# Kernel optimization log

Hardware: AMD Instinct MI355X
Metric: run time of the kernel (lower is better)

## Reference

```python
import jax, jax.numpy as jnp
import numpy as np

D_HID = 512          # RAECell output dim (nn.Linear(1024, 512))
DEPTH = 16           # internal levels -> 2**16 leaves, 131071 nodes


def _levels(left, right, leaf, root):
    """Group internal nodes by depth via host-side BFS (tree topology is static)."""
    levels = []
    frontier = [int(root)]
    while frontier:
        internal = [n for n in frontier if not leaf[n]]
        if internal:
            levels.append(np.asarray(internal, dtype=np.int32))
        frontier = [c for n in internal for c in (int(left[n]), int(right[n]))]
    return levels


def setup_inputs() -> dict:
    key = jax.random.key(0)
    n_leaves = 2 ** DEPTH
    n_nodes = 2 * n_leaves - 1
    first_leaf = n_leaves - 1
    idx = np.arange(n_nodes)
    # complete binary tree in heap layout
    left = np.where(idx < first_leaf, 2 * idx + 1, 0).astype(np.int64)
    right = np.where(idx < first_leaf, 2 * idx + 2, 0).astype(np.int64)
    is_leaf = (idx >= first_leaf).astype(np.int64)
    k1, k2, k3 = jax.random.split(key, 3)
    inp = jax.random.normal(k1, (n_nodes, D_HID), jnp.float32)
    W = jax.random.normal(k2, (D_HID, 2 * D_HID), jnp.float32) * (1.0 / np.sqrt(2 * D_HID))
    b = jax.random.normal(k3, (D_HID,), jnp.float32) * 0.01
    return {
        "left": jnp.asarray(left),
        "right": jnp.asarray(right),
        "is_leaf": jnp.asarray(is_leaf),
        "inp": inp,
        "root": 0,
        "W": W,
        "b": b,
    }


def reference(left, right, is_leaf, inp, root, W, b):
    # Tree indices are static -> pull to host once and batch the recursion
    # level-by-level (replaces the Python recursion + per-node tiny kernels
    # of the original with log2(N) batched concat+GEMM+tanh steps).
    l = np.asarray(left)
    r = np.asarray(right)
    leaf = np.asarray(is_leaf).astype(bool)
    levels = _levels(l, r, leaf, root)
    H = inp  # [n_nodes, 512]; leaf rows are the inputs, internal rows get overwritten bottom-up
    for lvl in reversed(levels):
        a = H[l[lvl]]              # [m, 512] left children
        c = H[r[lvl]]              # [m, 512] right children
        x = jnp.concatenate([a, c], axis=1)          # [m, 1024] == torch.cat((a, b))
        H = H.at[jnp.asarray(lvl)].set(jnp.tanh(x @ W.T + b))
    return H[int(root)]
```

## Files before the change

kernel.cpp:

```cpp
#include <hip/hip_runtime.h>
#include <hip/hip_fp16.h>

typedef _Float16 half8 __attribute__((ext_vector_type(8)));
typedef float f32x4 __attribute__((ext_vector_type(4)));

#define KDIM 1024
#define NDIM 512

#define GLOAD_LDS16(g, l) __builtin_amdgcn_global_load_lds(                 \
    (const __attribute__((address_space(1))) void*)(g),                     \
    (__attribute__((address_space(3))) void*)(l), 16, 0, 0)

__global__ __launch_bounds__(256, 2)
void rae_level_gemm_h(const _Float16* __restrict__ X, const _Float16* __restrict__ Wh,
                      const float* __restrict__ bias, _Float16* __restrict__ Yh)
{
    __shared__ _Float16 Xs[128 * 64];
    __shared__ _Float16 Ws[128 * 64];

    const int tid  = threadIdx.x;
    const int lane = tid & 63;
    const int wave = tid >> 6;
    const int wm = wave >> 1;
    const int wn = wave & 1;
    const int lrow = lane & 15;
    const int lq   = lane >> 4;

    const int brow = blockIdx.x * 128;
    const int bcol = blockIdx.y * 128;

    const int sr = tid >> 3;
    const int su = (((tid & 7) ^ (sr & 7)) << 3);

    const _Float16* xbase = X  + (size_t)(brow + sr) * KDIM + su;
    const _Float16* wbase = Wh + (size_t)(bcol + sr) * KDIM + su;

    f32x4 acc[4][4] = {};

    for (int k0 = 0; k0 < KDIM; k0 += 64) {
        __syncthreads();
        GLOAD_LDS16(xbase + k0,             Xs + tid * 8);
        GLOAD_LDS16(xbase + k0 + 32 * KDIM, Xs + tid * 8 + 2048);
        GLOAD_LDS16(xbase + k0 + 64 * KDIM, Xs + tid * 8 + 4096);
        GLOAD_LDS16(xbase + k0 + 96 * KDIM, Xs + tid * 8 + 6144);
        GLOAD_LDS16(wbase + k0,             Ws + tid * 8);
        GLOAD_LDS16(wbase + k0 + 32 * KDIM, Ws + tid * 8 + 2048);
        GLOAD_LDS16(wbase + k0 + 64 * KDIM, Ws + tid * 8 + 4096);
        GLOAD_LDS16(wbase + k0 + 96 * KDIM, Ws + tid * 8 + 6144);
        __syncthreads();

        #pragma unroll
        for (int ks = 0; ks < 2; ++ks) {
            half8 af[4], bf[4];
            #pragma unroll
            for (int i = 0; i < 4; ++i) {
                const int R = wm * 64 + i * 16 + lrow;
                const int phys = (ks * 4 + lq) ^ (R & 7);
                af[i] = *(const half8*)&Xs[R * 64 + phys * 8];
            }
            #pragma unroll
            for (int j = 0; j < 4; ++j) {
                const int R = wn * 64 + j * 16 + lrow;
                const int phys = (ks * 4 + lq) ^ (R & 7);
                bf[j] = *(const half8*)&Ws[R * 64 + phys * 8];
            }
            #pragma unroll
            for (int i = 0; i < 4; ++i)
                #pragma unroll
                for (int j = 0; j < 4; ++j)
                    acc[i][j] = __builtin_amdgcn_mfma_f32_16x16x32_f16(af[i], bf[j], acc[i][j], 0, 0, 0);
        }
    }

    #pragma unroll
    for (int j = 0; j < 4; ++j) {
        const int col = bcol + wn * 64 + j * 16 + lrow;
        const float bv = bias[col];
        #pragma unroll
        for (int i = 0; i < 4; ++i) {
            const int rbase = brow + wm * 64 + i * 16 + lq * 4;
            #pragma unroll
            for (int r = 0; r < 4; ++r)
                Yh[(size_t)(rbase + r) * NDIM + col] = (_Float16)tanhf(acc[i][j][r] + bv);
        }
    }
}

__device__ __forceinline__ void grid_barrier(unsigned* bar, unsigned nb)
{
    __syncthreads();
    if (threadIdx.x == 0) {
        __threadfence();
        unsigned* cnt = bar;
        unsigned* gen = bar + 32;
        unsigned g = __hip_atomic_load(gen, __ATOMIC_RELAXED, __HIP_MEMORY_SCOPE_AGENT);
        if (__hip_atomic_fetch_add(cnt, 1u, __ATOMIC_ACQ_REL, __HIP_MEMORY_SCOPE_AGENT) == nb - 1u) {
            __hip_atomic_store(cnt, 0u, __ATOMIC_RELAXED, __HIP_MEMORY_SCOPE_AGENT);
            __hip_atomic_store(gen, g + 1u, __ATOMIC_RELEASE, __HIP_MEMORY_SCOPE_AGENT);
        } else {
            while (__hip_atomic_load(gen, __ATOMIC_RELAXED, __HIP_MEMORY_SCOPE_AGENT) == g) {}
        }
        __threadfence();
    }
    __syncthreads();
}

#define TAIL_BK 256
#define TLD 264

__global__ __launch_bounds__(256, 1)
void rae_tail(const _Float16* __restrict__ Wh, const float* __restrict__ bias,
              _Float16* __restrict__ Hh, float* __restrict__ out,
              unsigned* __restrict__ bar)
{
    __shared__ _Float16 Xs[128 * TLD];
    __shared__ _Float16 Ws[64 * TLD];

    const int tid  = threadIdx.x;
    const int lane = tid & 63;
    const int wave = tid >> 6;
    const int lrow = lane & 15;
    const int lq   = lane >> 4;
    const int col0 = blockIdx.x * 64;

    const _Float16* wbase = Wh + (size_t)(col0 + (tid >> 2)) * KDIM + (size_t)((tid & 3) * 64);
    _Float16* wlds = Ws + (tid >> 2) * TLD + (tid & 3) * 64;

    const int xrow = tid >> 1;
    const int xseg = (tid & 1) * 128;

    for (int d = 7; d >= 0; --d) {
        const int m = 1 << d;
        const _Float16* X = Hh + (size_t)((2 << d) - 1) * NDIM;
        _Float16* Y = Hh + (size_t)((1 << d) - 1) * NDIM;

        f32x4 acc[2][4] = {};

        for (int k0 = 0; k0 < KDIM; k0 += TAIL_BK) {
            __syncthreads();
            {
                const _Float16* g = wbase + k0;
                #pragma unroll
                for (int j = 0; j < 8; ++j)
                    *(half8*)(wlds + j * 8) = *(const half8*)(g + j * 8);
            }
            if (xrow < m) {
                const _Float16* g = X + (size_t)xrow * KDIM + k0 + xseg;
                _Float16* l = Xs + xrow * TLD + xseg;
                #pragma unroll
                for (int j = 0; j < 16; ++j)
                    *(half8*)(l + j * 8) = *(const half8*)(g + j * 8);
            }
            __syncthreads();

            if (wave * 32 < m) {
                #pragma unroll
                for (int ks = 0; ks < TAIL_BK; ks += 32) {
                    half8 af[2], bf[4];
                    #pragma unroll
                    for (int i = 0; i < 2; ++i)
                        af[i] = *(const half8*)&Xs[(wave * 32 + i * 16 + lrow) * TLD + ks + lq * 8];
                    #pragma unroll
                    for (int j = 0; j < 4; ++j)
                        bf[j] = *(const half8*)&Ws[(j * 16 + lrow) * TLD + ks + lq * 8];
                    #pragma unroll
                    for (int i = 0; i < 2; ++i)
                        #pragma unroll
                        for (int j = 0; j < 4; ++j)
                            acc[i][j] = __builtin_amdgcn_mfma_f32_16x16x32_f16(af[i], bf[j], acc[i][j], 0, 0, 0);
                }
            }
        }

        if (wave * 32 < m) {
            #pragma unroll
            for (int j = 0; j < 4; ++j) {
                const int col = col0 + j * 16 + lrow;
                const float bv = bias[col];
                #pragma unroll
                for (int i = 0; i < 2; ++i) {
                    const int rbase = wave * 32 + i * 16 + lq * 4;
                    #pragma unroll
                    for (int r = 0; r < 4; ++r) {
                        const int row = rbase + r;
                        if (row < m) {
                            const float v = tanhf(acc[i][j][r] + bv);
                            if (d == 0) out[col] = v;
                            else Y[(size_t)row * NDIM + col] = (_Float16)v;
                        }
                    }
                }
            }
        }
        grid_barrier(bar, 8);
    }
}

__global__ void convert_w(const float* __restrict__ W, _Float16* __restrict__ Wh)
{
    const int i = blockIdx.x * 256 + threadIdx.x;
    const float4 v = ((const float4*)W)[i];
    _Float16 o[4] = {(_Float16)v.x, (_Float16)v.y, (_Float16)v.z, (_Float16)v.w};
    *(float2*)(Wh + (size_t)i * 4) = *(float2*)o;
}

__global__ void convert_leaves(const float* __restrict__ inp, _Float16* __restrict__ Hh)
{
    const size_t i = (size_t)blockIdx.x * 256 + threadIdx.x;
    const float4 v = ((const float4*)(inp + (size_t)65535 * NDIM))[i];
    _Float16 o[4] = {(_Float16)v.x, (_Float16)v.y, (_Float16)v.z, (_Float16)v.w};
    *(float2*)(Hh + (size_t)65535 * NDIM + i * 4) = *(float2*)o;
}

extern "C" void kernel_launch(void* const* d_in, const int* in_sizes, int n_in,
                              void* d_out, int out_size, void* d_ws, size_t ws_size,
                              hipStream_t stream)
{
    const float* inp  = (const float*)d_in[3];
    const float* W    = (const float*)d_in[5];
    const float* bias = (const float*)d_in[6];
    float* out = (float*)d_out;

    _Float16* Wh  = (_Float16*)d_ws;
    unsigned* bar = (unsigned*)((char*)d_ws + (1 << 20));
    _Float16* Hh  = (_Float16*)((char*)d_ws + (2 << 20));

    hipMemsetAsync(bar, 0, 256, stream);
    convert_w<<<512, 256, 0, stream>>>(W, Wh);
    convert_leaves<<<32768, 256, 0, stream>>>(inp, Hh);

    for (int d = 15; d >= 8; --d) {
        const int m = 1 << d;
        const _Float16* Xp = Hh + (size_t)((2 << d) - 1) * NDIM;
        _Float16* Yp = Hh + (size_t)((1 << d) - 1) * NDIM;
        rae_level_gemm_h<<<dim3(m / 128, 4), 256, 0, stream>>>(Xp, Wh, bias, Yp);
    }

    rae_tail<<<8, 256, 0, stream>>>(Wh, bias, Hh, out, bar);
}
```

Measured before the change: 675.1 us.

## Fuse leaf fp32 conversion into first level GEMM and widen persistent tail

Removes the separate leaf conversion kernel: the deepest level now reads fp32 leaves directly, converting them to fp16 on the way into LDS. This avoids writing and re-reading 64K fp16 rows. The persistent tail kernel now starts at depth 10 with 32 blocks instead of 8. It keeps a full 64-column strip of W resident in LDS and reads activations straight from global memory, which removes three GEMM launches. The costs are synchronous non-async X loads in the first level and more grid-barrier participants with little parallel work per level.

```diff
diff --git a/kernel.cpp b/kernel.cpp
--- a/kernel.cpp
+++ b/kernel.cpp
@@ -86,6 +86,89 @@
     }
 }
 
+__global__ __launch_bounds__(256, 2)
+void rae_level15_f32(const float* __restrict__ Xf, const _Float16* __restrict__ Wh,
+                     const float* __restrict__ bias, _Float16* __restrict__ Yh)
+{
+    __shared__ _Float16 Xs[128 * 64];
+    __shared__ _Float16 Ws[128 * 64];
+
+    const int tid  = threadIdx.x;
+    const int lane = tid & 63;
+    const int wave = tid >> 6;
+    const int wm = wave >> 1;
+    const int wn = wave & 1;
+    const int lrow = lane & 15;
+    const int lq   = lane >> 4;
+
+    const int brow = blockIdx.x * 128;
+    const int bcol = blockIdx.y * 128;
+
+    const int sr = tid >> 3;
+    const int su = (((tid & 7) ^ (sr & 7)) << 3);
+
+    const float*    xbase = Xf + (size_t)(brow + sr) * KDIM + su;
+    const _Float16* wbase = Wh + (size_t)(bcol + sr) * KDIM + su;
+
+    f32x4 acc[4][4] = {};
+
+    for (int k0 = 0; k0 < KDIM; k0 += 64) {
+        __syncthreads();
+        GLOAD_LDS16(wbase + k0,             Ws + tid * 8);
+        GLOAD_LDS16(wbase + k0 + 32 * KDIM, Ws + tid * 8 + 2048);
+        GLOAD_LDS16(wbase + k0 + 64 * KDIM, Ws + tid * 8 + 4096);
+        GLOAD_LDS16(wbase + k0 + 96 * KDIM, Ws + tid * 8 + 6144);
+        #pragma unroll
+        for (int c = 0; c < 4; ++c) {
+            const float4* g = (const float4*)(xbase + k0 + (size_t)c * 32 * KDIM);
+            const float4 aa = g[0];
+            const float4 bb = g[1];
+            half8 h;
+            h[0] = (_Float16)aa.x; h[1] = (_Float16)aa.y;
+            h[2] = (_Float16)aa.z; h[3] = (_Float16)aa.w;
+            h[4] = (_Float16)bb.x; h[5] = (_Float16)bb.y;
+            h[6] = (_Float16)bb.z; h[7] = (_Float16)bb.w;
+            *(half8*)(Xs + tid * 8 + c * 2048) = h;
+        }
+        __syncthreads();
+
+        #pragma unroll
+        for (int ks = 0; ks < 2; ++ks) {
+            half8 af[4], bf[4];
+            #pragma unroll
+            for (int i = 0; i < 4; ++i) {
+                const int R = wm * 64 + i * 16 + lrow;
+                const int phys = (ks * 4 + lq) ^ (R & 7);
+                af[i] = *(const half8*)&Xs[R * 64 + phys * 8];
+            }
+            #pragma unroll
+            for (int j = 0; j < 4; ++j) {
+                const int R = wn * 64 + j * 16 + lrow;
+                const int phys = (ks * 4 + lq) ^ (R & 7);
+                bf[j] = *(const half8*)&Ws[R * 64 + phys * 8];
+            }
+            #pragma unroll
+            for (int i = 0; i < 4; ++i)
+                #pragma unroll
+                for (int j = 0; j < 4; ++j)
+                    acc[i][j] = __builtin_amdgcn_mfma_f32_16x16x32_f16(af[i], bf[j], acc[i][j], 0, 0, 0);
+        }
+    }
+
+    #pragma unroll
+    for (int j = 0; j < 4; ++j) {
+        const int col = bcol + wn * 64 + j * 16 + lrow;
+        const float bv = bias[col];
+        #pragma unroll
+        for (int i = 0; i < 4; ++i) {
+            const int rbase = brow + wm * 64 + i * 16 + lq * 4;
+            #pragma unroll
+            for (int r = 0; r < 4; ++r)
+                Yh[(size_t)(rbase + r) * NDIM + col] = (_Float16)tanhf(acc[i][j][r] + bv);
+        }
+    }
+}
+
 __device__ __forceinline__ void grid_barrier(unsigned* bar, unsigned nb)
 {
     __syncthreads();
@@ -105,94 +188,91 @@
     __syncthreads();
 }
 
-#define TAIL_BK 256
-#define TLD 264
+#define TWLD 1032
+
+template<int NF>
+__device__ __forceinline__ void tail_level(
+    int d, const _Float16* __restrict__ Hh, float* __restrict__ out,
+    const float* __restrict__ bias, const _Float16* Ws,
+    int col0, int wstrip, int lrow, int lq, _Float16* __restrict__ Y)
+{
+    const int m = 1 << d;
+    const _Float16* X = Hh + ((size_t)(2 << d) - 1) * NDIM;
+    const int rbase0 = wstrip * (NF * 16);
+    if (NF == 1 && rbase0 >= m) return;
+
+    f32x4 acc[NF][4] = {};
+
+    #pragma unroll
+    for (int ks = 0; ks < 32; ++ks) {
+        half8 af[NF], bf[4];
+        #pragma unroll
+        for (int i = 0; i < NF; ++i)
+            af[i] = *(const half8*)(X + (size_t)(rbase0 + i * 16 + lrow) * KDIM + ks * 32 + lq * 8);
+        #pragma unroll
+        for (int j = 0; j < 4; ++j)
+            bf[j] = *(const half8*)(Ws + (j * 16 + lrow) * TWLD + ks * 32 + lq * 8);
+        #pragma unroll
+        for (int i = 0; i < NF; ++i)
+            #pragma unroll
+            for (int j = 0; j < 4; ++j)
+                acc[i][j] = __builtin_amdgcn_mfma_f32_16x16x32_f16(af[i], bf[j], acc[i][j], 0, 0, 0);
+    }
+
+    #pragma unroll
+    for (int j = 0; j < 4; ++j) {
+        const int col = col0 + j * 16 + lrow;
+        const float bv = bias[col];
+        #pragma unroll
+        for (int i = 0; i < NF; ++i) {
+            #pragma unroll
+            for (int r = 0; r < 4; ++r) {
+                const int row = rbase0 + i * 16 + lq * 4 + r;
+                if (row < m) {
+                    const float v = tanhf(acc[i][j][r] + bv);
+                    if (d == 0) out[col] = v;
+                    else Y[(size_t)row * NDIM + col] = (_Float16)v;
+                }
+            }
+        }
+    }
+}
 
 __global__ __launch_bounds__(256, 1)
 void rae_tail(const _Float16* __restrict__ Wh, const float* __restrict__ bias,
               _Float16* __restrict__ Hh, float* __restrict__ out,
               unsigned* __restrict__ bar)
 {
-    __shared__ _Float16 Xs[128 * TLD];
-    __shared__ _Float16 Ws[64 * TLD];
+    __shared__ _Float16 Ws[64 * TWLD];
 
     const int tid  = threadIdx.x;
     const int lane = tid & 63;
     const int wave = tid >> 6;
     const int lrow = lane & 15;
     const int lq   = lane >> 4;
-    const int col0 = blockIdx.x * 64;
-
-    const _Float16* wbase = Wh + (size_t)(col0 + (tid >> 2)) * KDIM + (size_t)((tid & 3) * 64);
-    _Float16* wlds = Ws + (tid >> 2) * TLD + (tid & 3) * 64;
-
-    const int xrow = tid >> 1;
-    const int xseg = (tid & 1) * 128;
-
-    for (int d = 7; d >= 0; --d) {
-        const int m = 1 << d;
-        const _Float16* X = Hh + (size_t)((2 << d) - 1) * NDIM;
-        _Float16* Y = Hh + (size_t)((1 << d) - 1) * NDIM;
-
-        f32x4 acc[2][4] = {};
-
-        for (int k0 = 0; k0 < KDIM; k0 += TAIL_BK) {
-            __syncthreads();
-            {
-                const _Float16* g = wbase + k0;
-                #pragma unroll
-                for (int j = 0; j < 8; ++j)
-                    *(half8*)(wlds + j * 8) = *(const half8*)(g + j * 8);
-            }
-            if (xrow < m) {
-                const _Float16* g = X + (size_t)xrow * KDIM + k0 + xseg;
-                _Float16* l = Xs + xrow * TLD + xseg;
-                #pragma unroll
-                for (int j = 0; j < 16; ++j)
-                    *(half8*)(l + j * 8) = *(const half8*)(g + j * 8);
-            }
-            __syncthreads();
-
-            if (wave * 32 < m) {
-                #pragma unroll
-                for (int ks = 0; ks < TAIL_BK; ks += 32) {
-                    half8 af[2], bf[4];
-                    #pragma unroll
-                    for (int i = 0; i < 2; ++i)
-                        af[i] = *(const half8*)&Xs[(wave * 32 + i * 16 + lrow) * TLD + ks + lq * 8];
-                    #pragma unroll
-                    for (int j = 0; j < 4; ++j)
-                        bf[j] = *(const half8*)&Ws[(j * 16 + lrow) * TLD + ks + lq * 8];
-                    #pragma unroll
-                    for (int i = 0; i < 2; ++i)
-                        #pragma unroll
-                        for (int j = 0; j < 4; ++j)
-                            acc[i][j] = __builtin_amdgcn_mfma_f32_16x16x32_f16(af[i], bf[j], acc[i][j], 0, 0, 0);
-                }
-            }
-        }
-
-        if (wave * 32 < m) {
-            #pragma unroll
-            for (int j = 0; j < 4; ++j) {
-                const int col = col0 + j * 16 + lrow;
-                const float bv = bias[col];
-                #pragma unroll
-                for (int i = 0; i < 2; ++i) {
-                    const int rbase = wave * 32 + i * 16 + lq * 4;
-                    #pragma unroll
-                    for (int r = 0; r < 4; ++r) {
-                        const int row = rbase + r;
-                        if (row < m) {
-                            const float v = tanhf(acc[i][j][r] + bv);
-                            if (d == 0) out[col] = v;
-                            else Y[(size_t)row * NDIM + col] = (_Float16)v;
-                        }
-                    }
-                }
-            }
-        }
-        grid_barrier(bar, 8);
+    const int strip = blockIdx.x & 7;
+    const int rgrp  = blockIdx.x >> 3;
+    const int col0  = strip * 64;
+    const int wstrip = rgrp * 4 + wave;
+
+    {
+        const _Float16* g = Wh + (size_t)(col0 + (tid >> 2)) * KDIM + (tid & 3) * 256;
+        _Float16* l = Ws + (tid >> 2) * TWLD + (tid & 3) * 256;
+        #pragma unroll
+        for (int j = 0; j < 32; ++j)
+            *(half8*)(l + j * 8) = *(const half8*)(g + j * 8);
+    }
+    __syncthreads();
+
+    for (int d = 10; d >= 0; --d) {
+        _Float16* Y = Hh + ((size_t)(1 << d) - 1) * NDIM;
+        if (d == 10)
+            tail_level<4>(d, Hh, out, bias, Ws, col0, wstrip, lrow, lq, Y);
+        else if (d == 9)
+            tail_level<2>(d, Hh, out, bias, Ws, col0, wstrip, lrow, lq, Y);
+        else
+            tail_level<1>(d, Hh, out, bias, Ws, col0, wstrip, lrow, lq, Y);
+        if (d) grid_barrier(bar, 32);
     }
 }
 
@@ -204,14 +284,6 @@
     *(float2*)(Wh + (size_t)i * 4) = *(float2*)o;
 }
 
-__global__ void convert_leaves(const float* __restrict__ inp, _Float16* __restrict__ Hh)
-{
-    const size_t i = (size_t)blockIdx.x * 256 + threadIdx.x;
-    const float4 v = ((const float4*)(inp + (size_t)65535 * NDIM))[i];
-    _Float16 o[4] = {(_Float16)v.x, (_Float16)v.y, (_Float16)v.z, (_Float16)v.w};
-    *(float2*)(Hh + (size_t)65535 * NDIM + i * 4) = *(float2*)o;
-}
-
 extern "C" void kernel_launch(void* const* d_in, const int* in_sizes, int n_in,
                               void* d_out, int out_size, void* d_ws, size_t ws_size,
                               hipStream_t stream)
@@ -227,14 +299,16 @@
 
     hipMemsetAsync(bar, 0, 256, stream);
     convert_w<<<512, 256, 0, stream>>>(W, Wh);
-    convert_leaves<<<32768, 256, 0, stream>>>(inp, Hh);
-
-    for (int d = 15; d >= 8; --d) {
+
+    rae_level15_f32<<<dim3(256, 4), 256, 0, stream>>>(
+        inp + (size_t)65535 * NDIM, Wh, bias, Hh + (size_t)32767 * NDIM);
+
+    for (int d = 14; d >= 11; --d) {
         const int m = 1 << d;
         const _Float16* Xp = Hh + (size_t)((2 << d) - 1) * NDIM;
         _Float16* Yp = Hh + (size_t)((1 << d) - 1) * NDIM;
         rae_level_gemm_h<<<dim3(m / 128, 4), 256, 0, stream>>>(Xp, Wh, bias, Yp);
     }
 
-    rae_tail<<<8, 256, 0, stream>>>(Wh, bias, Hh, out, bar);
-}
+    rae_tail<<<32, 256, 0, stream>>>(Wh, bias, Hh, out, bar);
+}
```

Measured after the change: 640.2 us. 5.2% less time.
